# Kernel tuning notes

Measured on AMD Instinct MI355X. Metric: run time of the kernel, lower is better.

The kernel has to match this reference:

```python
import jax, jax.numpy as jnp
import numpy as np

HIDDEN = 1024
HEADS = 16
D_HEAD = HIDDEN // HEADS  # 64
N = 2048


def setup_inputs() -> dict:
    key = jax.random.key(0)
    ks = jax.random.split(key, 12)
    s = 1.0 / np.sqrt(HIDDEN)
    return {
        "q": jax.random.normal(ks[0], (N, HIDDEN), jnp.float32),
        "k": jax.random.normal(ks[1], (N, HIDDEN), jnp.float32),
        "v": jax.random.normal(ks[2], (N, HIDDEN), jnp.float32),
        "attn_bias": jax.random.normal(ks[3], (HEADS, 1, N, N), jnp.float32),
        "Wq": jax.random.normal(ks[4], (HIDDEN, HIDDEN), jnp.float32) * s,
        "bq": jax.random.normal(ks[5], (HIDDEN,), jnp.float32) * s,
        "Wk": jax.random.normal(ks[6], (HIDDEN, HIDDEN), jnp.float32) * s,
        "bk": jax.random.normal(ks[7], (HIDDEN,), jnp.float32) * s,
        "Wv": jax.random.normal(ks[8], (HIDDEN, HIDDEN), jnp.float32) * s,
        "bv": jax.random.normal(ks[9], (HIDDEN,), jnp.float32) * s,
        "Wo": jax.random.normal(ks[10], (HIDDEN, HIDDEN), jnp.float32) * s,
        "bo": jax.random.normal(ks[11], (HIDDEN,), jnp.float32) * s,
    }


def reference(q, k, v, attn_bias, Wq, bq, Wk, bk, Wv, bv, Wo, bo):
    # q,k,v: [N, hidden]; attn_bias: [H, 1, N, N]. Attention runs over the
    # node axis (dim 0 in the torch code), inner seq dim is 1 (squeezed).
    n = q.shape[0]
    scale = D_HEAD ** -0.5
    qh = (q @ Wq.T + bq).reshape(n, HEADS, D_HEAD).transpose(1, 0, 2)  # [H,N,d]
    kh = (k @ Wk.T + bk).reshape(n, HEADS, D_HEAD).transpose(1, 0, 2)  # [H,N,d]
    vh = (v @ Wv.T + bv).reshape(n, HEADS, D_HEAD).transpose(1, 0, 2)  # [H,N,d]
    scores = jnp.einsum('hnd,hmd->hnm', qh * scale, kh) + attn_bias[:, 0]  # [H,N,N]
    attn = jax.nn.softmax(scores, axis=-1)
    ctx = jnp.einsum('hnm,hmd->hnd', attn, vh)            # [H,N,d]
    ctx = ctx.transpose(1, 0, 2).reshape(n, HEADS * D_HEAD)  # [N,hidden]
    return ctx @ Wo.T + bo
```

## Files before the change

kernel.cpp:

```cpp
#include <hip/hip_runtime.h>
#include <type_traits>
#include <utility>

#define NT 2048
#define HD 1024
#define NHEAD 16
#define DHEAD 64
#define LOG2E 1.44269504f

typedef float f32x4 __attribute__((ext_vector_type(4)));
typedef __bf16 b16x8 __attribute__((ext_vector_type(8)));
typedef short s16x8 __attribute__((ext_vector_type(8)));
typedef unsigned short u16x8 __attribute__((ext_vector_type(8)));
typedef unsigned short u16x4 __attribute__((ext_vector_type(4)));

template <typename V, typename = void>
struct mfma_takes : std::false_type {};
template <typename V>
struct mfma_takes<V, std::void_t<decltype(__builtin_amdgcn_mfma_f32_16x16x32_bf16(
                         std::declval<V>(), std::declval<V>(), std::declval<f32x4>(), 0, 0, 0))>>
    : std::true_type {};

template <typename V>
__device__ __forceinline__ f32x4 mfma_impl(V a, V b, f32x4 c) {
  return __builtin_amdgcn_mfma_f32_16x16x32_bf16(a, b, c, 0, 0, 0);
}

__device__ __forceinline__ f32x4 mfma_bf16(u16x8 a, u16x8 b, f32x4 c) {
  using V = typename std::conditional<mfma_takes<b16x8>::value, b16x8, s16x8>::type;
  return mfma_impl<V>(__builtin_bit_cast(V, a), __builtin_bit_cast(V, b), c);
}

__device__ __forceinline__ unsigned short f2bf(float f) {
  unsigned int u = __builtin_bit_cast(unsigned int, f);
  return (unsigned short)((u + 0x7FFFu + ((u >> 16) & 1u)) >> 16);
}

__device__ __forceinline__ void gload16(const unsigned short* g, unsigned short* l) {
  __builtin_amdgcn_global_load_lds(
      (__attribute__((address_space(1))) void*)(void*)(g),
      (__attribute__((address_space(3))) void*)(void*)(l), 16, 0, 0);
}

__device__ __forceinline__ void barrier_pinned() {
  __builtin_amdgcn_sched_barrier(0);
  __builtin_amdgcn_s_barrier();
  __builtin_amdgcn_sched_barrier(0);
}
#define WAIT_VM6() asm volatile("s_waitcnt vmcnt(6)" ::: "memory")
#define WAIT_VM0() asm volatile("s_waitcnt vmcnt(0)" ::: "memory")
#define WAIT_LGKM0() asm volatile("s_waitcnt lgkmcnt(0)" ::: "memory")

__global__ __launch_bounds__(256) void cvt_bf16(
    const float* __restrict__ s0, const float* __restrict__ s1, const float* __restrict__ s2,
    const float* __restrict__ s3, const float* __restrict__ s4, const float* __restrict__ s5,
    const float* __restrict__ s6,
    unsigned short* __restrict__ d0, unsigned short* __restrict__ d1, unsigned short* __restrict__ d2,
    unsigned short* __restrict__ d3, unsigned short* __restrict__ d4, unsigned short* __restrict__ d5,
    unsigned short* __restrict__ d6) {
  const int seg = blockIdx.y;
  const float* s;
  unsigned short* d;
  switch (seg) {
    case 0: s = s0; d = d0; break;
    case 1: s = s1; d = d1; break;
    case 2: s = s2; d = d2; break;
    case 3: s = s3; d = d3; break;
    case 4: s = s4; d = d4; break;
    case 5: s = s5; d = d5; break;
    default: s = s6; d = d6; break;
  }
  const int n = (seg < 3) ? NT * HD : HD * HD;
  for (int i = blockIdx.x * 2048 + threadIdx.x * 8; i < n; i += gridDim.x * 2048) {
    f32x4 f0 = *reinterpret_cast<const f32x4*>(&s[i]);
    f32x4 f1 = *reinterpret_cast<const f32x4*>(&s[i + 4]);
    u16x8 o;
#pragma unroll
    for (int e = 0; e < 4; ++e) { o[e] = f2bf(f0[e]); o[e + 4] = f2bf(f1[e]); }
    *reinterpret_cast<u16x8*>(&d[i]) = o;
  }
}

__device__ __forceinline__ void gemm64x128(
    const unsigned short* __restrict__ A, const unsigned short* __restrict__ B,
    int n0, int m0,
    unsigned short* As0, unsigned short* As1,
    unsigned short* Bs0, unsigned short* Bs1, f32x4 acc[2][4]) {
  const int tid = threadIdx.x;
  const int lane = tid & 63;
  const int wr = (tid >> 6) >> 1, wc = (tid >> 6) & 1;
  const int srow = tid >> 3;
  const int scol = (((tid & 7) ^ (srow & 7)) << 3);

  auto stage = [&](int kt, unsigned short* as, unsigned short* bs) {
#pragma unroll
    for (int p = 0; p < 2; ++p)
      gload16(&A[(size_t)(n0 + p * 32 + srow) * HD + kt + scol], as + p * 2048 + tid * 8);
#pragma unroll
    for (int p = 0; p < 4; ++p)
      gload16(&B[(size_t)(m0 + p * 32 + srow) * HD + kt + scol], bs + p * 2048 + tid * 8);
  };
  auto comp = [&](const unsigned short* as, const unsigned short* bs) {
#pragma unroll
    for (int ks = 0; ks < 2; ++ks) {
      const int q = ks * 4 + (lane >> 4);
      u16x8 a[2], b[4];
#pragma unroll
      for (int i = 0; i < 2; ++i) {
        const int row = wr * 32 + i * 16 + (lane & 15);
        a[i] = *reinterpret_cast<const u16x8*>(&as[row * 64 + ((q ^ (row & 7)) << 3)]);
      }
#pragma unroll
      for (int j = 0; j < 4; ++j) {
        const int row = wc * 64 + j * 16 + (lane & 15);
        b[j] = *reinterpret_cast<const u16x8*>(&bs[row * 64 + ((q ^ (row & 7)) << 3)]);
      }
#pragma unroll
      for (int i = 0; i < 2; ++i)
#pragma unroll
        for (int j = 0; j < 4; ++j)
          acc[i][j] = mfma_bf16(a[i], b[j], acc[i][j]);
    }
  };

  stage(0, As0, Bs0);
  stage(64, As1, Bs1);
#pragma unroll 1
  for (int s = 0; s < 14; ++s) {
    WAIT_VM6();
    barrier_pinned();
    if (s & 1) comp(As1, Bs1); else comp(As0, Bs0);
    barrier_pinned();
    if (s & 1) stage((s + 2) * 64, As1, Bs1);
    else       stage((s + 2) * 64, As0, Bs0);
  }
  WAIT_VM6();
  barrier_pinned();
  comp(As0, Bs0);
  WAIT_VM0();
  barrier_pinned();
  comp(As1, Bs1);
}

__global__ __launch_bounds__(256) void proj_gemm(
    const unsigned short* __restrict__ qb, const unsigned short* __restrict__ kb,
    const unsigned short* __restrict__ vb,
    const unsigned short* __restrict__ Wqb, const unsigned short* __restrict__ Wkb,
    const unsigned short* __restrict__ Wvb,
    const float* __restrict__ bq, const float* __restrict__ bk, const float* __restrict__ bv,
    unsigned short* __restrict__ Qh, unsigned short* __restrict__ Kh,
    unsigned short* __restrict__ Vt) {
  const int L = blockIdx.x;
  const int m = L / 96;
  const int c = L % 96;
  const int z = c / 32;
  const int n = c % 32;
  const int n0 = n * 64, m0 = m * 128;

  const unsigned short* A = (z == 0) ? qb : (z == 1) ? kb : vb;
  const unsigned short* B = (z == 0) ? Wqb : (z == 1) ? Wkb : Wvb;
  const float* bias = (z == 0) ? bq : (z == 1) ? bk : bv;

  __shared__ unsigned short As0[64 * 64], As1[64 * 64];
  __shared__ unsigned short Bs0[128 * 64], Bs1[128 * 64];

  const int tid = threadIdx.x;
  const int lane = tid & 63;
  const int wr = (tid >> 6) >> 1, wc = (tid >> 6) & 1;

  f32x4 acc[2][4] = {};
  gemm64x128(A, B, n0, m0, As0, As1, Bs0, Bs1, acc);

  const int rgrp = (lane >> 4) * 4;
  const float scale = (z == 0) ? 0.125f * LOG2E : 1.0f;
#pragma unroll
  for (int i = 0; i < 2; ++i) {
    const int nb = n0 + wr * 32 + i * 16 + rgrp;
#pragma unroll
    for (int j = 0; j < 4; ++j) {
      const int mcol = m0 + wc * 64 + j * 16 + (lane & 15);
      const float bb = bias[mcol];
      if (z == 2) {
        u16x4 pk;
#pragma unroll
        for (int r = 0; r < 4; ++r) pk[r] = f2bf(acc[i][j][r] + bb);
        *reinterpret_cast<u16x4*>(&Vt[(size_t)mcol * NT + nb]) = pk;
      } else {
        unsigned short* dst = (z == 0) ? Qh : Kh;
#pragma unroll
        for (int r = 0; r < 4; ++r)
          dst[(size_t)(nb + r) * HD + mcol] = f2bf((acc[i][j][r] + bb) * scale);
      }
    }
  }
}

__global__ __launch_bounds__(256) void attn_kernel(
    const unsigned short* __restrict__ Qh, const unsigned short* __restrict__ Kh,
    const unsigned short* __restrict__ Vt, const float* __restrict__ bias,
    unsigned short* __restrict__ ctx) {
  const int id = blockIdx.x;
  const int xcd = id & 7, slot = id >> 3;
  const int h = xcd * 2 + (slot >> 5);
  const int q0 = (slot & 31) * 64;
  const int tid = threadIdx.x;
  const int lane = tid & 63;
  const int wave = tid >> 6;

  __shared__ unsigned short Ks[128][72];
  __shared__ unsigned short Vs[64][136];
  __shared__ unsigned short Ps[4][16][136];

  u16x8 qf[2];
  {
    const int qrow = q0 + wave * 16 + (lane & 15);
    const int db = (lane >> 4) * 8;
    qf[0] = *reinterpret_cast<const u16x8*>(&Qh[(size_t)qrow * HD + h * DHEAD + db]);
    qf[1] = *reinterpret_cast<const u16x8*>(&Qh[(size_t)qrow * HD + h * DHEAD + 32 + db]);
  }

  f32x4 oacc[4] = {};
  float mrun[4], lrun[4];
#pragma unroll
  for (int r = 0; r < 4; ++r) { mrun[r] = -3.0e38f; lrun[r] = 0.f; }

  const float* bias_h = bias + (size_t)h * NT * NT;
  const int qlrow = q0 + wave * 16 + (lane >> 4) * 4;

  const int ksr = tid >> 3, ksc = (tid & 7) << 3;
  const int vsd = tid >> 2, vsc = (tid & 3) << 3;
  const unsigned short* Kbase = Kh + h * DHEAD;
  const unsigned short* Vbase = Vt + (size_t)(h * DHEAD + vsd) * NT;

  float br[8][4];
  {
    const float* bp = bias_h + (size_t)qlrow * NT + (lane & 15);
#pragma unroll
    for (int j = 0; j < 8; ++j)
#pragma unroll
      for (int r = 0; r < 4; ++r) br[j][r] = bp[(size_t)r * NT + j * 16];
  }
#pragma unroll
  for (int p = 0; p < 4; ++p)
    *reinterpret_cast<u16x8*>(&Ks[ksr + p * 32][ksc]) =
        *reinterpret_cast<const u16x8*>(&Kbase[(size_t)(ksr + p * 32) * HD + ksc]);
#pragma unroll
  for (int p = 0; p < 4; ++p)
    *reinterpret_cast<u16x8*>(&Vs[vsd][vsc + p * 32]) =
        *reinterpret_cast<const u16x8*>(&Vbase[vsc + p * 32]);
  WAIT_LGKM0();
  barrier_pinned();

#pragma unroll 1
  for (int t = 0; t < NT / 128; ++t) {
    f32x4 s[8] = {};
#pragma unroll
    for (int ks = 0; ks < 2; ++ks) {
      const int kcol = ks * 32 + (lane >> 4) * 8;
#pragma unroll
      for (int j = 0; j < 8; ++j) {
        u16x8 kf = *reinterpret_cast<const u16x8*>(&Ks[j * 16 + (lane & 15)][kcol]);
        s[j] = mfma_bf16(qf[ks], kf, s[j]);
      }
    }
#pragma unroll
    for (int j = 0; j < 8; ++j)
#pragma unroll
      for (int r = 0; r < 4; ++r) s[j][r] = fmaf(br[j][r], LOG2E, s[j][r]);

    const bool more = (t + 1 < NT / 128);
    u16x8 kpre[4], vpre[4];
    if (more) {
      const int kt2 = (t + 1) * 128;
      const float* bp = bias_h + (size_t)qlrow * NT + kt2 + (lane & 15);
#pragma unroll
      for (int j = 0; j < 8; ++j)
#pragma unroll
        for (int r = 0; r < 4; ++r) br[j][r] = bp[(size_t)r * NT + j * 16];
#pragma unroll
      for (int p = 0; p < 4; ++p)
        kpre[p] = *reinterpret_cast<const u16x8*>(&Kbase[(size_t)(kt2 + ksr + p * 32) * HD + ksc]);
#pragma unroll
      for (int p = 0; p < 4; ++p)
        vpre[p] = *reinterpret_cast<const u16x8*>(&Vbase[kt2 + vsc + p * 32]);
    }

    float mnew[4];
#pragma unroll
    for (int r = 0; r < 4; ++r) {
      float mx = s[0][r];
#pragma unroll
      for (int j = 1; j < 8; ++j) mx = fmaxf(mx, s[j][r]);
      mx = fmaxf(mx, __shfl_xor(mx, 1));
      mx = fmaxf(mx, __shfl_xor(mx, 2));
      mx = fmaxf(mx, __shfl_xor(mx, 4));
      mx = fmaxf(mx, __shfl_xor(mx, 8));
      mnew[r] = fmaxf(mrun[r], mx);
    }
#pragma unroll
    for (int r = 0; r < 4; ++r) {
      const float corr = exp2f(mrun[r] - mnew[r]);
      lrun[r] *= corr;
#pragma unroll
      for (int nd = 0; nd < 4; ++nd) oacc[nd][r] *= corr;
      mrun[r] = mnew[r];
    }
    float psum[4] = {0.f, 0.f, 0.f, 0.f};
#pragma unroll
    for (int j = 0; j < 8; ++j)
#pragma unroll
      for (int r = 0; r < 4; ++r) {
        const float p = exp2f(s[j][r] - mrun[r]);
        psum[r] += p;
        Ps[wave][(lane >> 4) * 4 + r][j * 16 + (lane & 15)] = f2bf(p);
      }
#pragma unroll
    for (int r = 0; r < 4; ++r) {
      float tsum = psum[r];
      tsum += __shfl_xor(tsum, 1);
      tsum += __shfl_xor(tsum, 2);
      tsum += __shfl_xor(tsum, 4);
      tsum += __shfl_xor(tsum, 8);
      lrun[r] += tsum;
    }

#pragma unroll
    for (int kk = 0; kk < 4; ++kk) {
      const int kcol = kk * 32 + (lane >> 4) * 8;
      u16x8 pa = *reinterpret_cast<const u16x8*>(&Ps[wave][lane & 15][kcol]);
#pragma unroll
      for (int nd = 0; nd < 4; ++nd) {
        u16x8 vb = *reinterpret_cast<const u16x8*>(&Vs[nd * 16 + (lane & 15)][kcol]);
        oacc[nd] = mfma_bf16(pa, vb, oacc[nd]);
      }
    }

    barrier_pinned();
    if (more) {
#pragma unroll
      for (int p = 0; p < 4; ++p)
        *reinterpret_cast<u16x8*>(&Ks[ksr + p * 32][ksc]) = kpre[p];
#pragma unroll
      for (int p = 0; p < 4; ++p)
        *reinterpret_cast<u16x8*>(&Vs[vsd][vsc + p * 32]) = vpre[p];
    }
    WAIT_LGKM0();
    barrier_pinned();
  }

#pragma unroll
  for (int nd = 0; nd < 4; ++nd) {
#pragma unroll
    for (int r = 0; r < 4; ++r) {
      const float val = oacc[nd][r] / lrun[r];
      ctx[(size_t)(qlrow + r) * HD + h * DHEAD + nd * 16 + (lane & 15)] = f2bf(val);
    }
  }
}

__global__ __launch_bounds__(256) void out_gemm(
    const unsigned short* __restrict__ Ain, const unsigned short* __restrict__ Wob,
    const float* __restrict__ bias, float* __restrict__ out) {
  const int L = blockIdx.x;
  const int m = L / 32;
  const int n = L % 32;
  const int n0 = n * 64, m0 = m * 128;

  __shared__ unsigned short As0[64 * 64], As1[64 * 64];
  __shared__ unsigned short Bs0[128 * 64], Bs1[128 * 64];

  const int tid = threadIdx.x;
  const int lane = tid & 63;
  const int wr = (tid >> 6) >> 1, wc = (tid >> 6) & 1;

  f32x4 acc[2][4] = {};
  gemm64x128(Ain, Wob, n0, m0, As0, As1, Bs0, Bs1, acc);

  const int rgrp = (lane >> 4) * 4;
#pragma unroll
  for (int i = 0; i < 2; ++i) {
    const int nb = n0 + wr * 32 + i * 16 + rgrp;
#pragma unroll
    for (int j = 0; j < 4; ++j) {
      const int mcol = m0 + wc * 64 + j * 16 + (lane & 15);
      const float bb = bias[mcol];
#pragma unroll
      for (int r = 0; r < 4; ++r)
        out[(size_t)(nb + r) * HD + mcol] = acc[i][j][r] + bb;
    }
  }
}

extern "C" void kernel_launch(void* const* d_in, const int* in_sizes, int n_in,
                              void* d_out, int out_size, void* d_ws, size_t ws_size,
                              hipStream_t stream) {
  const float* q  = (const float*)d_in[0];
  const float* k  = (const float*)d_in[1];
  const float* v  = (const float*)d_in[2];
  const float* ab = (const float*)d_in[3];
  const float* Wq = (const float*)d_in[4];
  const float* bq = (const float*)d_in[5];
  const float* Wk = (const float*)d_in[6];
  const float* bk = (const float*)d_in[7];
  const float* Wv = (const float*)d_in[8];
  const float* bv = (const float*)d_in[9];
  const float* Wo = (const float*)d_in[10];
  const float* bo = (const float*)d_in[11];

  unsigned short* qb  = (unsigned short*)d_ws;
  unsigned short* kb  = qb + (size_t)NT * HD;
  unsigned short* vb  = kb + (size_t)NT * HD;
  unsigned short* Wqb = vb + (size_t)NT * HD;
  unsigned short* Wkb = Wqb + (size_t)HD * HD;
  unsigned short* Wvb = Wkb + (size_t)HD * HD;
  unsigned short* Wob = Wvb + (size_t)HD * HD;
  unsigned short* Qh  = Wob + (size_t)HD * HD;
  unsigned short* Kh  = Qh + (size_t)NT * HD;
  unsigned short* Vt  = Kh + (size_t)NT * HD;
  unsigned short* ctx = Vt + (size_t)NT * HD;

  cvt_bf16<<<dim3(512, 7), 256, 0, stream>>>(q, k, v, Wq, Wk, Wv, Wo,
                                             qb, kb, vb, Wqb, Wkb, Wvb, Wob);
  proj_gemm<<<dim3(768), 256, 0, stream>>>(
      qb, kb, vb, Wqb, Wkb, Wvb, bq, bk, bv, Qh, Kh, Vt);
  attn_kernel<<<dim3(512), 256, 0, stream>>>(Qh, Kh, Vt, ab, ctx);
  out_gemm<<<dim3(256), 256, 0, stream>>>(ctx, Wob, bo, (float*)d_out);
}
```

Baseline: 124.5 us.

## Double-buffer attention K/V tiles with direct global-to-LDS loads and XOR swizzle

Replaces the register-staged K/V prefetch in the attention kernel with direct global-to-LDS loads (gload16) into two ping-pong LDS buffers. The next tile is issued at the top of each iteration, and one barrier per iteration replaces two. Padded LDS rows give way to an XOR-swizzled layout for the K, V and P tiles to avoid bank conflicts, and launch bounds now request 2 blocks per CU. This cuts register pressure and the store-to-LDS phase, at the cost of roughly doubled K/V LDS footprint, which could limit occupancy.

Measured after the change: 119.3 us. 4.2% less time.

```diff
diff --git a/kernel.cpp b/kernel.cpp
--- a/kernel.cpp
+++ b/kernel.cpp
@@ -195,7 +195,7 @@
   }
 }
 
-__global__ __launch_bounds__(256) void attn_kernel(
+__global__ __launch_bounds__(256, 2) void attn_kernel(
     const unsigned short* __restrict__ Qh, const unsigned short* __restrict__ Kh,
     const unsigned short* __restrict__ Vt, const float* __restrict__ bias,
     unsigned short* __restrict__ ctx) {
@@ -207,9 +207,9 @@
   const int lane = tid & 63;
   const int wave = tid >> 6;
 
-  __shared__ unsigned short Ks[128][72];
-  __shared__ unsigned short Vs[64][136];
-  __shared__ unsigned short Ps[4][16][136];
+  __shared__ unsigned short Ks0[128 * 64], Ks1[128 * 64];
+  __shared__ unsigned short Vs0[64 * 128], Vs1[64 * 128];
+  __shared__ unsigned short Ps[4 * 16 * 128];
 
   u16x8 qf[2];
   {
@@ -226,41 +226,58 @@
 
   const float* bias_h = bias + (size_t)h * NT * NT;
   const int qlrow = q0 + wave * 16 + (lane >> 4) * 4;
-
-  const int ksr = tid >> 3, ksc = (tid & 7) << 3;
-  const int vsd = tid >> 2, vsc = (tid & 3) << 3;
+  const float* bias_l = bias_h + (size_t)qlrow * NT + (lane & 15);
+
   const unsigned short* Kbase = Kh + h * DHEAD;
-  const unsigned short* Vbase = Vt + (size_t)(h * DHEAD + vsd) * NT;
+  const unsigned short* Vbase = Vt + (size_t)h * DHEAD * NT;
+
+  const int krow = tid >> 3;
+  const int kchk = tid & 7;
+  const int vrow = tid >> 4;
+  const int vchk = tid & 15;
+
+  auto stage = [&](int t, unsigned short* ks, unsigned short* vs) {
+    const int kt = t * 128;
+#pragma unroll
+    for (int p = 0; p < 4; ++p) {
+      const int r = p * 32 + krow;
+      gload16(&Kbase[(size_t)(kt + r) * HD + ((kchk ^ (r & 7)) << 3)], ks + p * 2048 + tid * 8);
+    }
+#pragma unroll
+    for (int p = 0; p < 4; ++p) {
+      const int r = p * 16 + vrow;
+      gload16(&Vbase[(size_t)r * NT + kt + ((vchk ^ (r & 7)) << 3)], vs + p * 2048 + tid * 8);
+    }
+  };
 
   float br[8][4];
-  {
-    const float* bp = bias_h + (size_t)qlrow * NT + (lane & 15);
-#pragma unroll
-    for (int j = 0; j < 8; ++j)
-#pragma unroll
-      for (int r = 0; r < 4; ++r) br[j][r] = bp[(size_t)r * NT + j * 16];
-  }
-#pragma unroll
-  for (int p = 0; p < 4; ++p)
-    *reinterpret_cast<u16x8*>(&Ks[ksr + p * 32][ksc]) =
-        *reinterpret_cast<const u16x8*>(&Kbase[(size_t)(ksr + p * 32) * HD + ksc]);
-#pragma unroll
-  for (int p = 0; p < 4; ++p)
-    *reinterpret_cast<u16x8*>(&Vs[vsd][vsc + p * 32]) =
-        *reinterpret_cast<const u16x8*>(&Vbase[vsc + p * 32]);
-  WAIT_LGKM0();
+#pragma unroll
+  for (int j = 0; j < 8; ++j)
+#pragma unroll
+    for (int r = 0; r < 4; ++r) br[j][r] = bias_l[(size_t)r * NT + j * 16];
+  stage(0, Ks0, Vs0);
+  WAIT_VM0();
   barrier_pinned();
+
+  unsigned short* const psw = Ps + wave * 2048;
 
 #pragma unroll 1
   for (int t = 0; t < NT / 128; ++t) {
+    const bool more = (t + 1 < NT / 128);
+    const unsigned short* ks = (t & 1) ? Ks1 : Ks0;
+    const unsigned short* vs = (t & 1) ? Vs1 : Vs0;
+
+    if (more) stage(t + 1, (t & 1) ? Ks0 : Ks1, (t & 1) ? Vs0 : Vs1);
+
     f32x4 s[8] = {};
 #pragma unroll
-    for (int ks = 0; ks < 2; ++ks) {
-      const int kcol = ks * 32 + (lane >> 4) * 8;
+    for (int kss = 0; kss < 2; ++kss) {
+      const int q = kss * 4 + (lane >> 4);
 #pragma unroll
       for (int j = 0; j < 8; ++j) {
-        u16x8 kf = *reinterpret_cast<const u16x8*>(&Ks[j * 16 + (lane & 15)][kcol]);
-        s[j] = mfma_bf16(qf[ks], kf, s[j]);
+        const int row = j * 16 + (lane & 15);
+        u16x8 kf = *reinterpret_cast<const u16x8*>(&ks[row * 64 + ((q ^ (row & 7)) << 3)]);
+        s[j] = mfma_bf16(qf[kss], kf, s[j]);
       }
     }
 #pragma unroll
@@ -268,21 +285,12 @@
 #pragma unroll
       for (int r = 0; r < 4; ++r) s[j][r] = fmaf(br[j][r], LOG2E, s[j][r]);
 
-    const bool more = (t + 1 < NT / 128);
-    u16x8 kpre[4], vpre[4];
     if (more) {
-      const int kt2 = (t + 1) * 128;
-      const float* bp = bias_h + (size_t)qlrow * NT + kt2 + (lane & 15);
+      const float* bp = bias_l + (size_t)(t + 1) * 128;
 #pragma unroll
       for (int j = 0; j < 8; ++j)
 #pragma unroll
         for (int r = 0; r < 4; ++r) br[j][r] = bp[(size_t)r * NT + j * 16];
-#pragma unroll
-      for (int p = 0; p < 4; ++p)
-        kpre[p] = *reinterpret_cast<const u16x8*>(&Kbase[(size_t)(kt2 + ksr + p * 32) * HD + ksc]);
-#pragma unroll
-      for (int p = 0; p < 4; ++p)
-        vpre[p] = *reinterpret_cast<const u16x8*>(&Vbase[kt2 + vsc + p * 32]);
     }
 
     float mnew[4];
@@ -307,13 +315,17 @@
     }
     float psum[4] = {0.f, 0.f, 0.f, 0.f};
 #pragma unroll
-    for (int j = 0; j < 8; ++j)
+    for (int j = 0; j < 8; ++j) {
+      const int chkbase = j * 2 + ((lane >> 3) & 1);
+      const int cofs = lane & 7;
 #pragma unroll
       for (int r = 0; r < 4; ++r) {
+        const int row = (lane >> 4) * 4 + r;
         const float p = exp2f(s[j][r] - mrun[r]);
         psum[r] += p;
-        Ps[wave][(lane >> 4) * 4 + r][j * 16 + (lane & 15)] = f2bf(p);
-      }
+        psw[row * 128 + ((chkbase ^ (row & 7)) << 3) + cofs] = f2bf(p);
+      }
+    }
 #pragma unroll
     for (int r = 0; r < 4; ++r) {
       float tsum = psum[r];
@@ -326,25 +338,18 @@
 
 #pragma unroll
     for (int kk = 0; kk < 4; ++kk) {
-      const int kcol = kk * 32 + (lane >> 4) * 8;
-      u16x8 pa = *reinterpret_cast<const u16x8*>(&Ps[wave][lane & 15][kcol]);
+      const int q = kk * 4 + (lane >> 4);
+      const int prow = lane & 15;
+      u16x8 pa = *reinterpret_cast<const u16x8*>(&psw[prow * 128 + ((q ^ (prow & 7)) << 3)]);
 #pragma unroll
       for (int nd = 0; nd < 4; ++nd) {
-        u16x8 vb = *reinterpret_cast<const u16x8*>(&Vs[nd * 16 + (lane & 15)][kcol]);
+        const int vr = nd * 16 + (lane & 15);
+        u16x8 vb = *reinterpret_cast<const u16x8*>(&vs[vr * 128 + ((q ^ (vr & 7)) << 3)]);
         oacc[nd] = mfma_bf16(pa, vb, oacc[nd]);
       }
     }
 
-    barrier_pinned();
-    if (more) {
-#pragma unroll
-      for (int p = 0; p < 4; ++p)
-        *reinterpret_cast<u16x8*>(&Ks[ksr + p * 32][ksc]) = kpre[p];
-#pragma unroll
-      for (int p = 0; p < 4; ++p)
-        *reinterpret_cast<u16x8*>(&Vs[vsd][vsc + p * 32]) = vpre[p];
-    }
-    WAIT_LGKM0();
+    WAIT_VM0();
     barrier_pinned();
   }
 
```
